# Performance work log

Measured on AMD Instinct MI355X. Metric: run time of the kernel, lower is better.

## Reference

```python
import jax, jax.numpy as jnp
import numpy as np

STRIDES = (4, 8, 16, 32, 64)
SIZES = (32.0, 64.0, 128.0, 256.0, 512.0)   # one anchor scale per FPN level
RATIOS = (0.5, 1.0, 2.0)                    # k = 3 anchors per location
FEAT_HW = ((256, 256), (128, 128), (64, 64), (32, 32), (16, 16))
TOPK = 1000          # pre_nms_top_k
NMS_THRES = 0.7      # nms_threshold
REG_W = (1.0, 1.0, 1.0, 1.0)
LOG_CLAMP = 4.0      # clamp on dw/dh before exp


def _gen_anchors():
    """generate_anchor_form: per-level [H,W,k,4] (cx,cy,w,h), flattened and concatenated -> [A,4]."""
    out = []
    for (H, W), s, sz in zip(FEAT_HW, STRIDES, SIZES):
        ys = (np.arange(H, dtype=np.float32) + 0.5) * s
        xs = (np.arange(W, dtype=np.float32) + 0.5) * s
        cy, cx = np.meshgrid(ys, xs, indexing='ij')
        r = np.asarray(RATIOS, dtype=np.float32)
        w = sz / np.sqrt(r)
        h = sz * np.sqrt(r)
        a = np.zeros((H, W, len(RATIOS), 4), np.float32)
        a[..., 0] = cx[..., None]
        a[..., 1] = cy[..., None]
        a[..., 2] = w
        a[..., 3] = h
        out.append(a.reshape(-1, 4))
    return jnp.asarray(np.concatenate(out, axis=0))  # [A,4]


def _iou_matrix(boxes):
    """boxes [K,4] in (cx,cy,w,h) -> pairwise IoU [K,K]."""
    x1 = boxes[:, 0] - boxes[:, 2] * 0.5
    y1 = boxes[:, 1] - boxes[:, 3] * 0.5
    x2 = boxes[:, 0] + boxes[:, 2] * 0.5
    y2 = boxes[:, 1] + boxes[:, 3] * 0.5
    area = (x2 - x1) * (y2 - y1)
    iw = jnp.clip(jnp.minimum(x2[:, None], x2[None, :]) - jnp.maximum(x1[:, None], x1[None, :]), 0.0)
    ih = jnp.clip(jnp.minimum(y2[:, None], y2[None, :]) - jnp.maximum(y1[:, None], y1[None, :]), 0.0)
    inter = iw * ih
    return inter / (area[:, None] + area[None, :] - inter + 1e-6)


def _nms_keep(boxes_sorted):
    """Greedy NMS over score-sorted boxes [K,4] -> keep mask [K] (bool)."""
    K = boxes_sorted.shape[0]
    iou = _iou_matrix(boxes_sorted)
    idxs = jnp.arange(K)

    def body(i, keep):
        sup = keep[i] & (iou[i] > NMS_THRES) & (idxs > i)
        return keep & (~sup)

    return jax.lax.fori_loop(0, K, body, jnp.ones((K,), bool))


def _anchor_preprocessing(cls_list, bbox_list):
    B = cls_list[0].shape[0]
    scores, deltas = [], []
    for c, b, (H, W) in zip(cls_list, bbox_list, FEAT_HW):
        # [B,k,H,W] -> [B,H*W*k]
        scores.append(c.transpose(0, 2, 3, 1).reshape(B, -1))
        # [B,4k,H,W] -> [B,H*W*k,4]
        deltas.append(b.reshape(B, len(RATIOS), 4, H, W).transpose(0, 3, 4, 1, 2).reshape(B, -1, 4))
    score = jax.nn.sigmoid(jnp.concatenate(scores, axis=1))  # [B,A]
    delta = jnp.concatenate(deltas, axis=1)                  # [B,A,4]

    anc = _gen_anchors()  # [A,4]
    wx, wy, ww, wh = REG_W
    cx = anc[:, 0] + (delta[..., 0] / wx) * anc[:, 2]
    cy = anc[:, 1] + (delta[..., 1] / wy) * anc[:, 3]
    w = anc[:, 2] * jnp.exp(jnp.clip(delta[..., 2] / ww, -LOG_CLAMP, LOG_CLAMP))
    h = anc[:, 3] * jnp.exp(jnp.clip(delta[..., 3] / wh, -LOG_CLAMP, LOG_CLAMP))
    post = jnp.stack([cx, cy, w, h], axis=-1)  # [B,A,4] decoded boxes

    # pre-NMS top-k per image
    _, topi = jax.lax.top_k(score, TOPK)                       # [B,K]
    boxes_k = jnp.take_along_axis(post, topi[..., None], axis=1)  # [B,K,4]
    keep_k = jax.vmap(_nms_keep)(boxes_k)                      # [B,K]

    A = score.shape[1]
    keep = jnp.zeros((B, A), bool).at[jnp.arange(B)[:, None], topi].set(keep_k)
    out = jnp.concatenate([post, score[..., None]], axis=-1) * keep[..., None].astype(post.dtype)
    return out, keep  # [B,A,5], [B,A]


def setup_inputs() -> dict:
    key = jax.random.key(0)
    ks = jax.random.split(key, 10)
    B = 16
    d = {}
    names_hw = list(zip(('p2', 'p3', 'p4', 'p5', 'p6'), FEAT_HW))
    for i, (n, (H, W)) in enumerate(names_hw):
        d['cls_' + n] = jax.random.normal(ks[i], (B, 3, H, W), jnp.float32)
        d['bbox_' + n] = jax.random.normal(ks[5 + i], (B, 12, H, W), jnp.float32) * 0.5
    return d


def reference(cls_p2, cls_p3, cls_p4, cls_p5, cls_p6,
              bbox_p2, bbox_p3, bbox_p4, bbox_p5, bbox_p6):
    return _anchor_preprocessing(
        [cls_p2, cls_p3, cls_p4, cls_p5, cls_p6],
        [bbox_p2, bbox_p3, bbox_p4, bbox_p5, bbox_p6])
```

## Files before the change

### kernel.cpp

```cpp
#include <hip/hip_runtime.h>
#include <cstdint>
#include <cstddef>

#define A_TOTAL 261888
#define NBATCH  16
#define KTOP    1000
#define CAP     2048
#define NMS_T   0.7f
#define F4_PER_IMG 65472
#define F4_PER_BLK 1023
#define STAGE_CAP 512

#define WS_HP    0
#define WS_CNT   1048640
#define WS_CAND  1048704
#define WS_IOUA  1310848
#define WS_POUT  1566848
#define WS_SOUT  1822848
#define WS_AOUT  1886848
#define WS_MASK  1950848

__constant__ float c_stride[5] = {4.f, 8.f, 16.f, 32.f, 64.f};
__constant__ float c_aw[5][3] = {
  {(float)(32.0 /0.707106769084930419921875),  32.f, (float)(32.0 /1.41421353816986083984375)},
  {(float)(64.0 /0.707106769084930419921875),  64.f, (float)(64.0 /1.41421353816986083984375)},
  {(float)(128.0/0.707106769084930419921875), 128.f, (float)(128.0/1.41421353816986083984375)},
  {(float)(256.0/0.707106769084930419921875), 256.f, (float)(256.0/1.41421353816986083984375)},
  {(float)(512.0/0.707106769084930419921875), 512.f, (float)(512.0/1.41421353816986083984375)}};
__constant__ float c_ah[5][3] = {
  {(float)(32.0 *0.707106769084930419921875),  32.f, (float)(32.0 *1.41421353816986083984375)},
  {(float)(64.0 *0.707106769084930419921875),  64.f, (float)(64.0 *1.41421353816986083984375)},
  {(float)(128.0*0.707106769084930419921875), 128.f, (float)(128.0*1.41421353816986083984375)},
  {(float)(256.0*0.707106769084930419921875), 256.f, (float)(256.0*1.41421353816986083984375)},
  {(float)(512.0*0.707106769084930419921875), 512.f, (float)(512.0*1.41421353816986083984375)}};

__device__ __forceinline__ void decompA(int a, int& l, int& i) {
  if (a < 245760) {
    if (a < 196608) { l = 0; i = a; } else { l = 1; i = a - 196608; }
  } else if (a < 258048) { l = 2; i = a - 245760; }
  else if (a < 261120)   { l = 3; i = a - 258048; }
  else                   { l = 4; i = a - 261120; }
}

__device__ __forceinline__ void decompE(int e, int& l, int& el) {
  if (e < 245760) {
    if (e < 196608) { l = 0; el = e; } else { l = 1; el = e - 196608; }
  } else if (e < 258048) { l = 2; el = e - 245760; }
  else if (e < 261120)   { l = 3; el = e - 258048; }
  else                   { l = 4; el = e - 261120; }
}

__device__ __forceinline__ int bin_of(float s) {
  int b = (int)(s * 16384.0f);
  return b > 16383 ? 16383 : (b < 0 ? 0 : b);
}

__device__ __forceinline__ float4 score4_at(const float* c0, const float* c1,
                                            const float* c2, const float* c3,
                                            const float* c4, int b, int f) {
  int l, off4;
  if (f < 49152) { l = 0; off4 = f; }
  else if (f < 61440) { l = 1; off4 = f - 49152; }
  else if (f < 64512) { l = 2; off4 = f - 61440; }
  else if (f < 65280) { l = 3; off4 = f - 64512; }
  else { l = 4; off4 = f - 65280; }
  int HW4x3 = 3 * (16384 >> (2 * l));
  const float4* p = (const float4*)((l == 0) ? c0 : (l == 1) ? c1 : (l == 2) ? c2
                                     : (l == 3) ? c3 : c4);
  float4 x = p[(size_t)b * HW4x3 + off4];
  float4 s;
  s.x = 1.0f / (1.0f + expf(-x.x));
  s.y = 1.0f / (1.0f + expf(-x.y));
  s.z = 1.0f / (1.0f + expf(-x.z));
  s.w = 1.0f / (1.0f + expf(-x.w));
  return s;
}

__device__ __forceinline__ void decode_box(const float* b0p, const float* b1p,
                                           const float* b2p, const float* b3p,
                                           const float* b4p, int b, int a,
                                           float& x1, float& y1, float& x2, float& y2,
                                           float& cx, float& cy, float& wb, float& hb) {
  int l, i; decompA(a, l, i);
  unsigned pix = (unsigned)i / 3u;
  int r = i - (int)pix * 3;
  int W = 256 >> l;
  int HW = 65536 >> (2 * l);
  int hh_i = (int)pix >> (8 - l);
  int ww_i = (int)pix & (W - 1);
  const float* bp = (l == 0) ? b0p : (l == 1) ? b1p : (l == 2) ? b2p : (l == 3) ? b3p : b4p;
  size_t base = (size_t)(b * 12 + r * 4) * HW + (size_t)pix;
  float d0 = bp[base];
  float d1 = bp[base + HW];
  float d2 = bp[base + 2 * (size_t)HW];
  float d3 = bp[base + 3 * (size_t)HW];
  float stride = c_stride[l];
  float cxa = ((float)ww_i + 0.5f) * stride;
  float cya = ((float)hh_i + 0.5f) * stride;
  float aw = c_aw[l][r], ah = c_ah[l][r];
  cx = cxa + d0 * aw;
  cy = cya + d1 * ah;
  wb = aw * expf(fminf(fmaxf(d2, -4.f), 4.f));
  hb = ah * expf(fminf(fmaxf(d3, -4.f), 4.f));
  x1 = cx - wb * 0.5f; x2 = cx + wb * 0.5f;
  y1 = cy - hb * 0.5f; y2 = cy + hb * 0.5f;
}

__global__ __launch_bounds__(256) void k_init(const float* c0, const float* c1,
                                              const float* c2, const float* c3,
                                              const float* c4,
                                              float4* o, int n4, int* cnt, int* hp) {
  __shared__ int lh[256];
  int bx = blockIdx.x, tid = threadIdx.x;
  int gstride = gridDim.x * 256;
  float4 z = make_float4(0.f, 0.f, 0.f, 0.f);
  for (int i = bx * 256 + tid; i < n4; i += gstride) o[i] = z;
  if (bx == 0 && tid < NBATCH) cnt[tid] = 0;
  if (bx < 1024) {
    lh[tid] = 0;
    __syncthreads();
    int b = bx >> 6, blk = bx & 63;
    int f0 = blk * F4_PER_BLK;
    #pragma unroll
    for (int it = 0; it < 4; it++) {
      int f = f0 + it * 256 + tid;
      if (f < f0 + F4_PER_BLK) {
        float4 s = score4_at(c0, c1, c2, c3, c4, b, f);
        atomicAdd(&lh[bin_of(s.x) >> 6], 1);
        atomicAdd(&lh[bin_of(s.y) >> 6], 1);
        atomicAdd(&lh[bin_of(s.z) >> 6], 1);
        atomicAdd(&lh[bin_of(s.w) >> 6], 1);
      }
    }
    __syncthreads();
    hp[(size_t)(b * 64 + blk) * 256 + tid] = lh[tid];
  }
}

__global__ __launch_bounds__(256) void k_compact(const float* c0, const float* c1,
                                                 const float* c2, const float* c3,
                                                 const float* c4, const int* hp,
                                                 int* cnt, unsigned long long* cand) {
  __shared__ int ch[256];
  __shared__ unsigned long long stage[STAGE_CAP];
  __shared__ int b0s, lc, gbase;
  int b = blockIdx.y, blk = blockIdx.x, tid = threadIdx.x;
  int s = 0;
  for (int k = 0; k < 64; k++) s += hp[(size_t)(b * 64 + k) * 256 + tid];
  ch[tid] = s;
  if (tid == 0) lc = 0;
  __syncthreads();
  if (tid == 0) {
    int acc = 0, cs = 0;
    for (int cb = 255; cb >= 0; cb--) {
      if (acc + ch[cb] >= KTOP) { cs = cb; break; }
      acc += ch[cb];
    }
    b0s = cs * 64;
  }
  __syncthreads();
  int B0v = b0s;
  int f0 = blk * F4_PER_BLK;
  #pragma unroll
  for (int it = 0; it < 4; it++) {
    int f = f0 + it * 256 + tid;
    if (f < f0 + F4_PER_BLK) {
      float4 sc4 = score4_at(c0, c1, c2, c3, c4, b, f);
      float sv[4] = {sc4.x, sc4.y, sc4.z, sc4.w};
      #pragma unroll
      for (int j = 0; j < 4; j++) {
        if (bin_of(sv[j]) >= B0v) {
          int e = f * 4 + j;
          int l, el; decompE(e, l, el);
          int shift = 16 - 2 * l;
          int r = el >> shift;
          int pix = el & ((1 << shift) - 1);
          int a = (e - el) + pix * 3 + r;
          int pos = atomicAdd(&lc, 1);
          if (pos < STAGE_CAP) {
            unsigned key = ~__float_as_uint(sv[j]);
            stage[pos] = ((unsigned long long)key << 32) | (unsigned)a;
          }
        }
      }
    }
  }
  __syncthreads();
  if (tid == 0) {
    int c = lc; if (c > STAGE_CAP) c = STAGE_CAP;
    lc = c;
    gbase = atomicAdd(&cnt[b], c);
  }
  __syncthreads();
  int c = lc, g0 = gbase;
  for (int t = tid; t < c; t += 256) {
    int gp = g0 + t;
    if (gp < CAP) cand[(size_t)b * CAP + gp] = stage[t];
  }
}

__global__ __launch_bounds__(64) void k_rank(const float* b0p, const float* b1p,
                                             const float* b2p, const float* b3p,
                                             const float* b4p,
                                             const unsigned long long* cand,
                                             const int* cnt,
                                             float4* iouA, float4* pout,
                                             float* sout, int* aout) {
  __shared__ unsigned long long sk[CAP];
  int b = blockIdx.y, g = blockIdx.x;
  int lane = threadIdx.x;
  int n = cnt[b]; if (n > CAP) n = CAP;
  for (int t = lane; t < CAP; t += 64)
    sk[t] = (t < n) ? cand[(size_t)b * CAP + t] : ~0ull;
  __syncthreads();
  int s0 = g * 128 + lane, s1 = s0 + 64;
  unsigned long long my0 = sk[s0], my1 = sk[s1];
  int r0 = 0, r1 = 0;
  #pragma unroll 4
  for (int j = 0; j < n; j++) {
    unsigned long long k = sk[j];
    r0 += (k < my0) ? 1 : 0;
    r1 += (k < my1) ? 1 : 0;
  }
  #pragma unroll
  for (int pass = 0; pass < 2; pass++) {
    int slot = pass == 0 ? s0 : s1;
    int r = pass == 0 ? r0 : r1;
    unsigned long long e = pass == 0 ? my0 : my1;
    if (slot < n && r < KTOP) {
      int a = (int)(unsigned)e;
      float sc = __uint_as_float(~(unsigned)(e >> 32));
      float x1, y1, x2, y2, cx, cy, wb, hb;
      decode_box(b0p, b1p, b2p, b3p, b4p, b, a, x1, y1, x2, y2, cx, cy, wb, hb);
      int o = b * KTOP + r;
      iouA[o] = make_float4(x1, y1, x2, y2);
      pout[o] = make_float4(cx, cy, wb, hb);
      sout[o] = sc;
      aout[o] = a;
    }
  }
}

__global__ __launch_bounds__(1024) void k_iou(const float4* iouA,
                                              unsigned long long* gmaskT) {
  __shared__ float4 bx[KTOP];
  int b = blockIdx.y;
  int tid = threadIdx.x;
  if (tid < KTOP) bx[tid] = iouA[b * KTOP + tid];
  __syncthreads();
  int row = blockIdx.x * 64 + (tid >> 4);
  int cc = tid & 15;
  if (row >= KTOP) return;
  float4 rb = bx[row];
  float rar = (rb.z - rb.x) * (rb.w - rb.y);
  unsigned long long bits = 0;
  int cbase = cc * 64;
  #pragma unroll 4
  for (int c = 0; c < 64; c++) {
    int col = cbase + c;
    if (col < KTOP && col != row) {
      float4 cb4 = bx[col];
      float iw = fminf(rb.z, cb4.z) - fmaxf(rb.x, cb4.x); iw = fmaxf(iw, 0.f);
      float ih = fminf(rb.w, cb4.w) - fmaxf(rb.y, cb4.y); ih = fmaxf(ih, 0.f);
      float inter = iw * ih;
      float car = (cb4.z - cb4.x) * (cb4.w - cb4.y);
      float iou = inter / (rar + car - inter + 1e-6f);
      if (iou > NMS_T) bits |= (1ull << c);
    }
  }
  gmaskT[((size_t)b * 16 + cc) * KTOP + row] = bits;
}

__global__ __launch_bounds__(1024) void k_greedy(const unsigned long long* gmaskT,
                                                 const float4* pout, const float* sout,
                                                 const int* aout,
                                                 float* out5, float* keepo) {
  __shared__ unsigned long long rem[16];
  __shared__ unsigned long long kept64[16];
  int b = blockIdx.x;
  int tid = threadIdx.x;
  if (tid < 16) rem[tid] = 0ull;
  __syncthreads();
  for (int c = 0; c < 16; c++) {
    if (tid < 64) {
      int j = tid;
      int row = c * 64 + j;
      unsigned long long w = 0ull;
      int sup = 1;
      if (row < KTOP) {
        w = gmaskT[((size_t)b * 16 + c) * KTOP + row];
        sup = (int)((rem[c] >> j) & 1ull);
      }
      for (int i = 0; i < 64; i++) {
        unsigned long long bal = __ballot(sup == 0);
        if (j > i && ((bal >> i) & 1ull) && ((w >> i) & 1ull)) sup = 1;
      }
      unsigned long long km = __ballot(sup == 0);
      if (j == 0) kept64[c] = km;
    }
    __syncthreads();
    {
      int wv = tid >> 6, i = tid & 63;
      unsigned long long km = kept64[c];
      int row = c * 64 + i;
      unsigned long long v = 0ull;
      if (row < KTOP && ((km >> i) & 1ull))
        v = gmaskT[((size_t)b * 16 + wv) * KTOP + row];
      for (int o = 32; o > 0; o >>= 1) v |= __shfl_xor(v, o, 64);
      if (i == 0) rem[wv] |= v;
    }
    __syncthreads();
  }
  if (tid < KTOP && ((kept64[tid >> 6] >> (tid & 63)) & 1ull)) {
    int o = b * KTOP + tid;
    float4 pq = pout[o];
    float sc = sout[o];
    int a = aout[o];
    size_t p = (size_t)b * A_TOTAL + (size_t)a;
    float* op = out5 + p * 5;
    op[0] = pq.x; op[1] = pq.y; op[2] = pq.z; op[3] = pq.w; op[4] = sc;
    keepo[p] = 1.0f;
  }
}

extern "C" void kernel_launch(void* const* d_in, const int* in_sizes, int n_in,
                              void* d_out, int out_size, void* d_ws, size_t ws_size,
                              hipStream_t stream) {
  const float *cls[5], *bbox[5];
  if (n_in >= 10 && in_sizes[1] == 4 * in_sizes[0]) {
    for (int l = 0; l < 5; l++) { cls[l] = (const float*)d_in[2*l]; bbox[l] = (const float*)d_in[2*l+1]; }
  } else {
    for (int l = 0; l < 5; l++) { cls[l] = (const float*)d_in[l]; bbox[l] = (const float*)d_in[5+l]; }
  }

  char* ws = (char*)d_ws;
  int* hp     = (int*)(ws + WS_HP);
  int* cnt    = (int*)(ws + WS_CNT);
  unsigned long long* cand = (unsigned long long*)(ws + WS_CAND);
  float4* iouA = (float4*)(ws + WS_IOUA);
  float4* pout = (float4*)(ws + WS_POUT);
  float*  sout = (float*)(ws + WS_SOUT);
  int*    aout = (int*)(ws + WS_AOUT);
  unsigned long long* gmaskT = (unsigned long long*)(ws + WS_MASK);

  float* out5  = (float*)d_out;
  float* keepo = out5 + (size_t)NBATCH * A_TOTAL * 5;

  k_init<<<4096, 256, 0, stream>>>(cls[0], cls[1], cls[2], cls[3], cls[4],
                                   (float4*)d_out, (NBATCH * A_TOTAL * 6) / 4,
                                   cnt, hp);
  dim3 g64(64, NBATCH);
  k_compact<<<g64, 256, 0, stream>>>(cls[0], cls[1], cls[2], cls[3], cls[4],
                                     hp, cnt, cand);
  dim3 gr(16, NBATCH);
  k_rank<<<gr, 64, 0, stream>>>(bbox[0], bbox[1], bbox[2], bbox[3], bbox[4],
                                cand, cnt, iouA, pout, sout, aout);
  dim3 gi(16, NBATCH);
  k_iou<<<gi, 1024, 0, stream>>>(iouA, gmaskT);
  k_greedy<<<NBATCH, 1024, 0, stream>>>(gmaskT, pout, sout, aout, out5, keepo);
}
```

Measured before the change: 335.6 us.

## Fuse IoU and greedy NMS, compute suppression lazily from kept rows only

Replaces the full 1000x1000 IoU bitmask kernel plus greedy kernel with one per-image NMS kernel. It computes only the diagonal 64x64 blocks up front and, after each chunk, recomputes IoU only against the rows that were kept. It also hoists the histogram threshold scan into a separate small kernel, so each compact block no longer re-sums 64 partial histograms. The cost is that the NMS work now runs on only 16 blocks with sequential chunk dependencies, and the stage count gains one launch.

```diff
diff --git a/kernel.cpp b/kernel.cpp
--- a/kernel.cpp
+++ b/kernel.cpp
@@ -12,13 +12,13 @@
 #define STAGE_CAP 512
 
 #define WS_HP    0
-#define WS_CNT   1048640
+#define WS_CNT   1048576
+#define WS_B0C   1048640
 #define WS_CAND  1048704
 #define WS_IOUA  1310848
 #define WS_POUT  1566848
 #define WS_SOUT  1822848
 #define WS_AOUT  1886848
-#define WS_MASK  1950848
 
 __constant__ float c_stride[5] = {4.f, 8.f, 16.f, 32.f, 64.f};
 __constant__ float c_aw[5][3] = {
@@ -137,29 +137,33 @@
   }
 }
 
-__global__ __launch_bounds__(256) void k_compact(const float* c0, const float* c1,
-                                                 const float* c2, const float* c3,
-                                                 const float* c4, const int* hp,
-                                                 int* cnt, unsigned long long* cand) {
+__global__ __launch_bounds__(256) void k_scan(const int* hp, int* b0c) {
   __shared__ int ch[256];
-  __shared__ unsigned long long stage[STAGE_CAP];
-  __shared__ int b0s, lc, gbase;
-  int b = blockIdx.y, blk = blockIdx.x, tid = threadIdx.x;
+  int b = blockIdx.x, t = threadIdx.x;
   int s = 0;
-  for (int k = 0; k < 64; k++) s += hp[(size_t)(b * 64 + k) * 256 + tid];
-  ch[tid] = s;
-  if (tid == 0) lc = 0;
-  __syncthreads();
-  if (tid == 0) {
+  for (int k = 0; k < 64; k++) s += hp[(size_t)(b * 64 + k) * 256 + t];
+  ch[t] = s;
+  __syncthreads();
+  if (t == 0) {
     int acc = 0, cs = 0;
     for (int cb = 255; cb >= 0; cb--) {
       if (acc + ch[cb] >= KTOP) { cs = cb; break; }
       acc += ch[cb];
     }
-    b0s = cs * 64;
-  }
-  __syncthreads();
-  int B0v = b0s;
+    b0c[b] = cs * 64;
+  }
+}
+
+__global__ __launch_bounds__(256) void k_compact(const float* c0, const float* c1,
+                                                 const float* c2, const float* c3,
+                                                 const float* c4, const int* b0c,
+                                                 int* cnt, unsigned long long* cand) {
+  __shared__ unsigned long long stage[STAGE_CAP];
+  __shared__ int lc, gbase;
+  int b = blockIdx.y, blk = blockIdx.x, tid = threadIdx.x;
+  if (tid == 0) lc = 0;
+  __syncthreads();
+  int B0v = b0c[b];
   int f0 = blk * F4_PER_BLK;
   #pragma unroll
   for (int it = 0; it < 4; it++) {
@@ -241,77 +245,81 @@
   }
 }
 
-__global__ __launch_bounds__(1024) void k_iou(const float4* iouA,
-                                              unsigned long long* gmaskT) {
+__global__ __launch_bounds__(1024) void k_nms(const float4* iouA, const float4* pout,
+                                              const float* sout, const int* aout,
+                                              float* out5, float* keepo) {
   __shared__ float4 bx[KTOP];
-  int b = blockIdx.y;
-  int tid = threadIdx.x;
-  if (tid < KTOP) bx[tid] = iouA[b * KTOP + tid];
-  __syncthreads();
-  int row = blockIdx.x * 64 + (tid >> 4);
-  int cc = tid & 15;
-  if (row >= KTOP) return;
-  float4 rb = bx[row];
-  float rar = (rb.z - rb.x) * (rb.w - rb.y);
-  unsigned long long bits = 0;
-  int cbase = cc * 64;
-  #pragma unroll 4
-  for (int c = 0; c < 64; c++) {
-    int col = cbase + c;
-    if (col < KTOP && col != row) {
-      float4 cb4 = bx[col];
-      float iw = fminf(rb.z, cb4.z) - fmaxf(rb.x, cb4.x); iw = fmaxf(iw, 0.f);
-      float ih = fminf(rb.w, cb4.w) - fmaxf(rb.y, cb4.y); ih = fmaxf(ih, 0.f);
-      float inter = iw * ih;
-      float car = (cb4.z - cb4.x) * (cb4.w - cb4.y);
-      float iou = inter / (rar + car - inter + 1e-6f);
-      if (iou > NMS_T) bits |= (1ull << c);
-    }
-  }
-  gmaskT[((size_t)b * 16 + cc) * KTOP + row] = bits;
-}
-
-__global__ __launch_bounds__(1024) void k_greedy(const unsigned long long* gmaskT,
-                                                 const float4* pout, const float* sout,
-                                                 const int* aout,
-                                                 float* out5, float* keepo) {
+  __shared__ unsigned long long diag[1024];
   __shared__ unsigned long long rem[16];
-  __shared__ unsigned long long kept64[16];
+  __shared__ unsigned long long kept64v[16];
   int b = blockIdx.x;
   int tid = threadIdx.x;
-  if (tid < 16) rem[tid] = 0ull;
-  __syncthreads();
+  int wv = tid >> 6, lane = tid & 63;
+  if (tid < KTOP) bx[tid] = iouA[b * KTOP + tid];
+  if (tid < 16) { rem[tid] = 0ull; kept64v[tid] = 0ull; }
+  __syncthreads();
+
+  int mycol = wv * 64 + lane;
+  bool colok = mycol < KTOP;
+  float4 cb = colok ? bx[mycol] : make_float4(0.f, 0.f, 0.f, 0.f);
+  float car = (cb.z - cb.x) * (cb.w - cb.y);
+
+  {
+    int rbase = wv * 64;
+    for (int i = 0; i < 64; i++) {
+      int row = rbase + i;
+      bool bit = false;
+      if (row < KTOP && colok && mycol != row) {
+        float4 rb = bx[row];
+        float rar = (rb.z - rb.x) * (rb.w - rb.y);
+        float iw = fminf(rb.z, cb.z) - fmaxf(rb.x, cb.x); iw = fmaxf(iw, 0.f);
+        float ih = fminf(rb.w, cb.w) - fmaxf(rb.y, cb.y); ih = fmaxf(ih, 0.f);
+        float inter = iw * ih;
+        float iou = inter / (rar + car - inter + 1e-6f);
+        bit = iou > NMS_T;
+      }
+      unsigned long long wbits = __ballot(bit);
+      if (lane == 0) diag[row] = wbits;
+    }
+  }
+  __syncthreads();
+
   for (int c = 0; c < 16; c++) {
-    if (tid < 64) {
-      int j = tid;
-      int row = c * 64 + j;
-      unsigned long long w = 0ull;
-      int sup = 1;
-      if (row < KTOP) {
-        w = gmaskT[((size_t)b * 16 + c) * KTOP + row];
-        sup = (int)((rem[c] >> j) & 1ull);
-      }
+    if (wv == 0) {
+      int row = c * 64 + lane;
+      unsigned long long w = diag[c * 64 + lane];
+      unsigned long long remc = rem[c];
+      int sup = (row < KTOP) ? (int)((remc >> lane) & 1ull) : 1;
       for (int i = 0; i < 64; i++) {
         unsigned long long bal = __ballot(sup == 0);
-        if (j > i && ((bal >> i) & 1ull) && ((w >> i) & 1ull)) sup = 1;
+        if (lane > i && ((bal >> i) & 1ull) && ((w >> i) & 1ull)) sup = 1;
       }
       unsigned long long km = __ballot(sup == 0);
-      if (j == 0) kept64[c] = km;
+      if (lane == 0) kept64v[c] = km;
     }
     __syncthreads();
-    {
-      int wv = tid >> 6, i = tid & 63;
-      unsigned long long km = kept64[c];
-      int row = c * 64 + i;
-      unsigned long long v = 0ull;
-      if (row < KTOP && ((km >> i) & 1ull))
-        v = gmaskT[((size_t)b * 16 + wv) * KTOP + row];
-      for (int o = 32; o > 0; o >>= 1) v |= __shfl_xor(v, o, 64);
-      if (i == 0) rem[wv] |= v;
+    if (c < 15) {
+      unsigned long long m = kept64v[c];
+      bool hit = false;
+      while (m) {
+        int r = __ffsll((unsigned long long)m) - 1;
+        m &= m - 1;
+        int row = c * 64 + r;
+        float4 rb = bx[row];
+        float rar = (rb.z - rb.x) * (rb.w - rb.y);
+        float iw = fminf(rb.z, cb.z) - fmaxf(rb.x, cb.x); iw = fmaxf(iw, 0.f);
+        float ih = fminf(rb.w, cb.w) - fmaxf(rb.y, cb.y); ih = fmaxf(ih, 0.f);
+        float inter = iw * ih;
+        float iou = inter / (rar + car - inter + 1e-6f);
+        if (colok && mycol != row && iou > NMS_T) hit = true;
+      }
+      unsigned long long wbits = __ballot(hit);
+      if (lane == 0) rem[wv] |= wbits;
     }
     __syncthreads();
   }
-  if (tid < KTOP && ((kept64[tid >> 6] >> (tid & 63)) & 1ull)) {
+
+  if (tid < KTOP && ((kept64v[tid >> 6] >> (tid & 63)) & 1ull)) {
     int o = b * KTOP + tid;
     float4 pq = pout[o];
     float sc = sout[o];
@@ -336,12 +344,12 @@
   char* ws = (char*)d_ws;
   int* hp     = (int*)(ws + WS_HP);
   int* cnt    = (int*)(ws + WS_CNT);
+  int* b0c    = (int*)(ws + WS_B0C);
   unsigned long long* cand = (unsigned long long*)(ws + WS_CAND);
   float4* iouA = (float4*)(ws + WS_IOUA);
   float4* pout = (float4*)(ws + WS_POUT);
   float*  sout = (float*)(ws + WS_SOUT);
   int*    aout = (int*)(ws + WS_AOUT);
-  unsigned long long* gmaskT = (unsigned long long*)(ws + WS_MASK);
 
   float* out5  = (float*)d_out;
   float* keepo = out5 + (size_t)NBATCH * A_TOTAL * 5;
@@ -349,13 +357,12 @@
   k_init<<<4096, 256, 0, stream>>>(cls[0], cls[1], cls[2], cls[3], cls[4],
                                    (float4*)d_out, (NBATCH * A_TOTAL * 6) / 4,
                                    cnt, hp);
+  k_scan<<<NBATCH, 256, 0, stream>>>(hp, b0c);
   dim3 g64(64, NBATCH);
   k_compact<<<g64, 256, 0, stream>>>(cls[0], cls[1], cls[2], cls[3], cls[4],
-                                     hp, cnt, cand);
+                                     b0c, cnt, cand);
   dim3 gr(16, NBATCH);
   k_rank<<<gr, 64, 0, stream>>>(bbox[0], bbox[1], bbox[2], bbox[3], bbox[4],
                                 cand, cnt, iouA, pout, sout, aout);
-  dim3 gi(16, NBATCH);
-  k_iou<<<gi, 1024, 0, stream>>>(iouA, gmaskT);
-  k_greedy<<<NBATCH, 1024, 0, stream>>>(gmaskT, pout, sout, aout, out5, keepo);
-}
+  k_nms<<<NBATCH, 1024, 0, stream>>>(iouA, pout, sout, aout, out5, keepo);
+}
```

Result: slower. 512.9 us (+52.8%).

## Split histogram scan into own kernel, rotate IoU columns, scalarize NMS greedy

Applied to the files above, without the earlier changes.

The per-image threshold scan moves out of k_compact into a separate small kernel, so the 64 compact blocks per image no longer each re-sum the 64 partial histograms. The IoU kernel rotates its column order per lane group to spread LDS bank accesses. The greedy NMS inner loop replaces 64 ballots with a scalar readlane-based sweep over diagonal masks prefetched into shared memory, and it skips the final reduction step. This adds one more kernel launch in exchange.

```diff
diff --git a/kernel.cpp b/kernel.cpp
--- a/kernel.cpp
+++ b/kernel.cpp
@@ -12,7 +12,8 @@
 #define STAGE_CAP 512
 
 #define WS_HP    0
-#define WS_CNT   1048640
+#define WS_CNT   1048576
+#define WS_B0C   1048640
 #define WS_CAND  1048704
 #define WS_IOUA  1310848
 #define WS_POUT  1566848
@@ -137,29 +138,33 @@
   }
 }
 
-__global__ __launch_bounds__(256) void k_compact(const float* c0, const float* c1,
-                                                 const float* c2, const float* c3,
-                                                 const float* c4, const int* hp,
-                                                 int* cnt, unsigned long long* cand) {
+__global__ __launch_bounds__(256) void k_scan(const int* hp, int* b0c) {
   __shared__ int ch[256];
-  __shared__ unsigned long long stage[STAGE_CAP];
-  __shared__ int b0s, lc, gbase;
-  int b = blockIdx.y, blk = blockIdx.x, tid = threadIdx.x;
+  int b = blockIdx.x, t = threadIdx.x;
   int s = 0;
-  for (int k = 0; k < 64; k++) s += hp[(size_t)(b * 64 + k) * 256 + tid];
-  ch[tid] = s;
-  if (tid == 0) lc = 0;
-  __syncthreads();
-  if (tid == 0) {
+  for (int k = 0; k < 64; k++) s += hp[(size_t)(b * 64 + k) * 256 + t];
+  ch[t] = s;
+  __syncthreads();
+  if (t == 0) {
     int acc = 0, cs = 0;
     for (int cb = 255; cb >= 0; cb--) {
       if (acc + ch[cb] >= KTOP) { cs = cb; break; }
       acc += ch[cb];
     }
-    b0s = cs * 64;
-  }
-  __syncthreads();
-  int B0v = b0s;
+    b0c[b] = cs * 64;
+  }
+}
+
+__global__ __launch_bounds__(256) void k_compact(const float* c0, const float* c1,
+                                                 const float* c2, const float* c3,
+                                                 const float* c4, const int* b0c,
+                                                 int* cnt, unsigned long long* cand) {
+  __shared__ unsigned long long stage[STAGE_CAP];
+  __shared__ int lc, gbase;
+  int b = blockIdx.y, blk = blockIdx.x, tid = threadIdx.x;
+  if (tid == 0) lc = 0;
+  __syncthreads();
+  int B0v = b0c[b];
   int f0 = blk * F4_PER_BLK;
   #pragma unroll
   for (int it = 0; it < 4; it++) {
@@ -257,7 +262,8 @@
   int cbase = cc * 64;
   #pragma unroll 4
   for (int c = 0; c < 64; c++) {
-    int col = cbase + c;
+    int cr = (c + cc) & 63;
+    int col = cbase + cr;
     if (col < KTOP && col != row) {
       float4 cb4 = bx[col];
       float iw = fminf(rb.z, cb4.z) - fmaxf(rb.x, cb4.x); iw = fmaxf(iw, 0.f);
@@ -265,7 +271,7 @@
       float inter = iw * ih;
       float car = (cb4.z - cb4.x) * (cb4.w - cb4.y);
       float iou = inter / (rar + car - inter + 1e-6f);
-      if (iou > NMS_T) bits |= (1ull << c);
+      if (iou > NMS_T) bits |= (1ull << cr);
     }
   }
   gmaskT[((size_t)b * 16 + cc) * KTOP + row] = bits;
@@ -275,43 +281,62 @@
                                                  const float4* pout, const float* sout,
                                                  const int* aout,
                                                  float* out5, float* keepo) {
+  __shared__ unsigned long long diag[1024];
   __shared__ unsigned long long rem[16];
-  __shared__ unsigned long long kept64[16];
+  __shared__ unsigned long long keptv[16];
   int b = blockIdx.x;
   int tid = threadIdx.x;
-  if (tid < 16) rem[tid] = 0ull;
-  __syncthreads();
+  int wv = tid >> 6, lane = tid & 63;
+  {
+    int row = wv * 64 + lane;
+    diag[tid] = (row < KTOP) ? gmaskT[((size_t)b * 16 + wv) * KTOP + row] : 0ull;
+  }
+  if (tid < 16) { rem[tid] = 0ull; keptv[tid] = 0ull; }
+  __syncthreads();
+
   for (int c = 0; c < 16; c++) {
-    if (tid < 64) {
-      int j = tid;
-      int row = c * 64 + j;
-      unsigned long long w = 0ull;
-      int sup = 1;
-      if (row < KTOP) {
-        w = gmaskT[((size_t)b * 16 + c) * KTOP + row];
-        sup = (int)((rem[c] >> j) & 1ull);
-      }
-      for (int i = 0; i < 64; i++) {
-        unsigned long long bal = __ballot(sup == 0);
-        if (j > i && ((bal >> i) & 1ull) && ((w >> i) & 1ull)) sup = 1;
-      }
-      unsigned long long km = __ballot(sup == 0);
-      if (j == 0) kept64[c] = km;
+    if (wv == 0) {
+      unsigned long long dw = diag[c * 64 + lane];
+      unsigned dlo = (unsigned)dw, dhi = (unsigned)(dw >> 32);
+      unsigned long long r0 = rem[c];
+      if (c == 15) r0 |= ~((1ull << 40) - 1);
+      unsigned slo = __builtin_amdgcn_readfirstlane((unsigned)r0);
+      unsigned shi = __builtin_amdgcn_readfirstlane((unsigned)(r0 >> 32));
+      unsigned klo = 0u, khi = 0u;
+      #pragma unroll
+      for (int i = 0; i < 32; i++) {
+        unsigned t = (~slo >> i) & 1u;
+        unsigned m = 0u - t;
+        klo |= t << i;
+        slo |= __builtin_amdgcn_readlane(dlo, i) & m;
+        shi |= __builtin_amdgcn_readlane(dhi, i) & m;
+      }
+      #pragma unroll
+      for (int i = 0; i < 32; i++) {
+        unsigned t = (~shi >> i) & 1u;
+        unsigned m = 0u - t;
+        khi |= t << i;
+        slo |= __builtin_amdgcn_readlane(dlo, 32 + i) & m;
+        shi |= __builtin_amdgcn_readlane(dhi, 32 + i) & m;
+      }
+      if (lane == 0) keptv[c] = ((unsigned long long)khi << 32) | klo;
     }
     __syncthreads();
-    {
-      int wv = tid >> 6, i = tid & 63;
-      unsigned long long km = kept64[c];
-      int row = c * 64 + i;
+    if (c < 15) {
+      unsigned long long km = keptv[c];
       unsigned long long v = 0ull;
-      if (row < KTOP && ((km >> i) & 1ull))
+      if ((km >> lane) & 1ull) {
+        int row = c * 64 + lane;
         v = gmaskT[((size_t)b * 16 + wv) * KTOP + row];
+      }
+      #pragma unroll
       for (int o = 32; o > 0; o >>= 1) v |= __shfl_xor(v, o, 64);
-      if (i == 0) rem[wv] |= v;
-    }
-    __syncthreads();
-  }
-  if (tid < KTOP && ((kept64[tid >> 6] >> (tid & 63)) & 1ull)) {
+      if (lane == 0) rem[wv] |= v;
+      __syncthreads();
+    }
+  }
+
+  if (tid < KTOP && ((keptv[tid >> 6] >> (tid & 63)) & 1ull)) {
     int o = b * KTOP + tid;
     float4 pq = pout[o];
     float sc = sout[o];
@@ -336,6 +361,7 @@
   char* ws = (char*)d_ws;
   int* hp     = (int*)(ws + WS_HP);
   int* cnt    = (int*)(ws + WS_CNT);
+  int* b0c    = (int*)(ws + WS_B0C);
   unsigned long long* cand = (unsigned long long*)(ws + WS_CAND);
   float4* iouA = (float4*)(ws + WS_IOUA);
   float4* pout = (float4*)(ws + WS_POUT);
@@ -349,9 +375,10 @@
   k_init<<<4096, 256, 0, stream>>>(cls[0], cls[1], cls[2], cls[3], cls[4],
                                    (float4*)d_out, (NBATCH * A_TOTAL * 6) / 4,
                                    cnt, hp);
+  k_scan<<<NBATCH, 256, 0, stream>>>(hp, b0c);
   dim3 g64(64, NBATCH);
   k_compact<<<g64, 256, 0, stream>>>(cls[0], cls[1], cls[2], cls[3], cls[4],
-                                     hp, cnt, cand);
+                                     b0c, cnt, cand);
   dim3 gr(16, NBATCH);
   k_rank<<<gr, 64, 0, stream>>>(bbox[0], bbox[1], bbox[2], bbox[3], bbox[4],
                                 cand, cnt, iouA, pout, sout, aout);
```

Result: faster. 284.2 us (-15.3%).
